# Kernel tuning notes

Hardware: AMD Instinct MI355X
Metric: run time of the kernel (lower is better)

## Reference

```python
import jax, jax.numpy as jnp
import numpy as np

NUM_T = 1000   # num_timesteps == timesteps -> skip = 1, seq = range(0, 1000)
ETA = 0.1
BETA_START, BETA_END = 1e-4, 0.02


def _ddim_schedule():
    # get_beta_schedule: linspace in float64, then cast
    betas = np.linspace(BETA_START, BETA_END, NUM_T, dtype=np.float64)
    # compute_alpha prepends beta=0 -> alpha_cumprod[0] = 1.0, indexed at t+1
    alph = np.concatenate([[1.0], np.cumprod(1.0 - betas)]).astype(np.float32)
    seq = np.arange(NUM_T)
    seq_next = np.concatenate([[-1], seq[:-1]])
    at = alph[seq + 1]
    at_next = alph[seq_next + 1]   # t=-1 -> alph[0] = 1.0
    # loop iterates reversed(seq) x reversed(seq_next)
    return (jnp.asarray(at[::-1].copy()),
            jnp.asarray(at_next[::-1].copy()),
            jnp.asarray(seq[::-1].copy(), dtype=jnp.int32))


def setup_inputs() -> dict:
    key = jax.random.key(0)
    k1, k2, k3, k4, k5 = jax.random.split(key, 5)
    n, c, s, h, w = 2, 3, 8, 64, 44
    return {
        "skes": jax.random.normal(k1, (n, c, s, h, w), dtype=jnp.float32),
        "sil_T": jax.random.normal(k2, (n * s, 1, h, w), dtype=jnp.float32),
        "w_skes": jax.random.normal(k3, (c,), dtype=jnp.float32),
        "w_sil": jax.random.normal(k4, (), dtype=jnp.float32),
        "t_scale": jax.random.normal(k5, (), dtype=jnp.float32),
    }


def reference(skes, sil_T, w_skes, w_sil, t_scale):
    n, c, s, h, w = skes.shape
    # rearrange 'n c s h w -> (n s) c h w'
    skes2 = jnp.transpose(skes, (0, 2, 1, 3, 4)).reshape(n * s, c, h, w)
    # surrogate denoiser condition: 1x1 channel projection of the skeleton maps
    cond = jnp.einsum('nchw,c->nhw', skes2, w_skes)[:, None]  # (n*s,1,h,w)
    at_r, atn_r, idx_r = _ddim_schedule()
    noise_key = jax.random.key(42)

    def model(sil_t, t_val):
        t_emb = t_scale * (t_val.astype(jnp.float32) / NUM_T)
        return jnp.tanh(cond + w_sil * sil_t + t_emb)

    def step(sil_t, x):
        at, atn, idx = x
        sil_0 = model(sil_t, idx)
        # NOTE: original uses the FIXED initial noise sil_T here (not sil_t)
        et = (sil_T - jnp.sqrt(at) * sil_0) / jnp.sqrt(1.0 - at)
        c1 = ETA * jnp.sqrt((1.0 - at / atn) * (1.0 - atn) / (1.0 - at))
        c2 = jnp.sqrt(jnp.maximum(1.0 - atn - c1 * c1, 0.0))
        noise = jax.random.normal(jax.random.fold_in(noise_key, idx),
                                  sil_T.shape, dtype=sil_T.dtype)
        sil_next = jnp.sqrt(atn) * sil_0 + c1 * noise + c2 * et
        return sil_next, sil_0

    _, preds = jax.lax.scan(step, sil_T, (at_r, atn_r, idx_r))
    # preds: (1000, n*s, 1, h, w) == stacked list of per-step sil_0 predictions
    return preds
```

## Files before the change

### kernel.cpp

```cpp
#include <hip/hip_runtime.h>
#include <cstdint>

#define NSTEP 1000
#define NELEM 45056
#define HW    2816
#define EPB   64
#define PW    7
#define BLK   ((PW + 1) * 64)
#define WIN   40
#define NWIN  (NSTEP / WIN)
#define NBUF  2
#define TABC_OFF 16384
#define WS_NEED  (TABC_OFF + NSTEP * 8)

struct AlphTab { float a[NSTEP + 1]; };

constexpr AlphTab make_alph() {
    AlphTab t{};
    t.a[0] = 1.0f;
    double alph = 1.0;
    const double start = 1e-4, stop = 0.02;
    const double step = (stop - start) / 999.0;
    for (int i = 0; i < NSTEP; ++i) {
        double beta = (i == NSTEP - 1) ? stop : ((double)i * step + start);
        alph *= (1.0 - beta);
        t.a[i + 1] = (float)alph;
    }
    return t;
}
constexpr AlphTab ALPH = make_alph();

__device__ __forceinline__ void tf20(uint32_t K0, uint32_t K1, uint32_t K2,
                                     uint32_t& x0, uint32_t& x1) {
    x0 += K0; x1 += K1;
#define TFR(r) { x0 += x1; x1 = ((x1 << r) | (x1 >> (32 - r))); x1 ^= x0; }
    TFR(13) TFR(15) TFR(26) TFR(6)
    x0 += K1; x1 += K2 + 1u;
    TFR(17) TFR(29) TFR(16) TFR(24)
    x0 += K2; x1 += K0 + 2u;
    TFR(13) TFR(15) TFR(26) TFR(6)
    x0 += K0; x1 += K1 + 3u;
    TFR(17) TFR(29) TFR(16) TFR(24)
    x0 += K1; x1 += K2 + 4u;
    TFR(13) TFR(15) TFR(26) TFR(6)
    x0 += K2; x1 += K0 + 5u;
#undef TFR
}

__device__ __forceinline__ float fast_tanh(float x) {
    const float e2 = __expf(x + x);
    const float r  = __builtin_amdgcn_rcpf(e2 + 1.0f);
    return fmaf(-2.0f, r, 1.0f);
}

__device__ __forceinline__ float bits_to_erfinv(uint32_t bits) {
    const float f2 = __uint_as_float((bits >> 9) | 0x3F800000u) - 1.0f;
    const float u  = f2 * 2.0f - 0.99999994f;
    const float t1 = (1.0f - u) * (1.0f + u);
    const float w  = __log2f(t1) * -0.6931472f;
    const bool  lt = w < 5.0f;

    const float wwn = w - 2.5f;
    float pn =           2.81022636e-08f;
    pn = fmaf(pn, wwn,   3.43273939e-07f);
    pn = fmaf(pn, wwn,  -3.5233877e-06f);
    pn = fmaf(pn, wwn,  -4.39150654e-06f);
    pn = fmaf(pn, wwn,   0.00021858087f);
    pn = fmaf(pn, wwn,  -0.00125372503f);
    pn = fmaf(pn, wwn,  -0.00417768164f);
    pn = fmaf(pn, wwn,   0.246640727f);
    pn = fmaf(pn, wwn,   1.50140941f);

    float p = pn;
    if (__any(!lt)) {
        const float sw  = __builtin_amdgcn_sqrtf(w);
        const float wwf = sw - 3.0f;
        float pf =           -0.000200214257f;
        pf = fmaf(pf, wwf,    0.000100950558f);
        pf = fmaf(pf, wwf,    0.00134934322f);
        pf = fmaf(pf, wwf,   -0.00367342844f);
        pf = fmaf(pf, wwf,    0.00573950773f);
        pf = fmaf(pf, wwf,   -0.0076224613f);
        pf = fmaf(pf, wwf,    0.00943887047f);
        pf = fmaf(pf, wwf,    1.00167406f);
        pf = fmaf(pf, wwf,    2.83297682f);
        p = lt ? pn : pf;
    }
    return p * u;
}

__global__ __launch_bounds__(256)
void setup_kernel(const float* __restrict__ tsc_p,
                  uint4* __restrict__ tabPg, uint2* __restrict__ tabCg) {
    const int k = (int)(blockIdx.x * 256u + threadIdx.x);
    if (k >= NSTEP) return;
    const float tsc = tsc_p[0];
    const float L2E2 = 2.8853900817779268f;
    const int t = 999 - k;
    const float at  = ALPH.a[t + 1];
    const float atn = ALPH.a[t];
    const float c1 = 0.1f * sqrtf((1.0f - at / atn) * (1.0f - atn) / (1.0f - at));
    const float c2 = sqrtf(fmaxf(1.0f - atn - c1 * c1, 0.0f));
    const float rs = 1.0f / sqrtf(1.0f - at);
    const float A  = sqrtf(atn) - c2 * sqrtf(at) * rs;
    const float e  = c2 * rs;
    const float temb = tsc * ((float)t / 1000.0f);
    uint32_t k0 = 0u, k1 = (uint32_t)t;
    tf20(0u, 42u, 0x1BD11BDAu ^ 42u, k0, k1);
    tabPg[k] = make_uint4(__float_as_uint(c1 * 1.4142135f),
                          __float_as_uint(e), k0, k1);
    tabCg[k] = make_uint2(__float_as_uint(A), __float_as_uint(temb * L2E2));
}

__device__ __forceinline__ void produce_window(const uint4* __restrict__ tabPg,
                                               float* __restrict__ db,
                                               int kbase, int wid, int lane,
                                               int j, float sT) {
    const int ks0 = __builtin_amdgcn_readfirstlane(kbase + wid);
#pragma unroll 2
    for (int s = 0, kk = wid; kk < WIN; ++s, kk += PW) {
        const uint4 ta = tabPg[ks0 + s * PW];
        uint32_t x0 = 0u, x1 = (uint32_t)j;
        tf20(ta.z, ta.w, ta.z ^ ta.w ^ 0x1BD11BDAu, x0, x1);
        const float ei = bits_to_erfinv(x0 ^ x1);
        db[kk * EPB + lane] =
            fmaf(__uint_as_float(ta.x), ei, __uint_as_float(ta.y) * sT);
    }
}

__global__ __launch_bounds__(BLK, 8)
void fused_kernel(const float* __restrict__ skes,
                  const float* __restrict__ silT,
                  const float* __restrict__ wskes,
                  const float* __restrict__ wsil_p,
                  const uint4* __restrict__ tabPg,
                  const uint2* __restrict__ tabCg,
                  float* __restrict__ out) {
    __shared__ __align__(16) float dbuf[NBUF][WIN][EPB];

    const int wid  = (int)(threadIdx.x >> 6);
    const int lane = (int)(threadIdx.x & 63);
    const int j    = (int)(blockIdx.x * EPB) + lane;

    const float sT = silT[j];

    float cc2 = 0.0f, ws2 = 0.0f, sil = 0.0f;
    if (wid == PW) {
        const float L2E2 = 2.8853900817779268f;
        const int ns = j / HW;
        const int hw = j - ns * HW;
        const int n  = ns >> 3;
        const int ss = ns & 7;
        const float* sk = skes + (size_t)((n * 3) * 8 + ss) * HW + hw;
        const float w0 = wskes[0], w1 = wskes[1], w2 = wskes[2];
        const float cond = fmaf(w2, sk[2 * 8 * HW], fmaf(w1, sk[8 * HW], w0 * sk[0]));
        cc2 = cond * L2E2;
        ws2 = wsil_p[0] * L2E2;
        sil = sT;
    }

    if (wid < PW) {
        produce_window(tabPg, &dbuf[0][0][0], 0, wid, lane, j, sT);
    }
    __syncthreads();

    float* op = out + j;

    for (int w = 0; w < NWIN; ++w) {
        if (wid < PW) {
            if (w + 1 < NWIN) {
                produce_window(tabPg, &dbuf[(w + 1) & (NBUF - 1)][0][0],
                               (w + 1) * WIN, wid, lane, j, sT);
            }
        } else {
            const float* db = &dbuf[w & (NBUF - 1)][0][0];
            const int ks0 = __builtin_amdgcn_readfirstlane(w * WIN);
#pragma unroll 1
            for (int g = 0; g < WIN / 8; ++g) {
                float d8[8]; uint2 t8[8];
#pragma unroll
                for (int i = 0; i < 8; ++i) {
                    d8[i] = db[(g * 8 + i) * EPB + lane];
                    t8[i] = tabCg[ks0 + g * 8 + i];
                }
#pragma unroll
                for (int i = 0; i < 8; ++i) {
                    const float A  = __uint_as_float(t8[i].x);
                    const float tb = __uint_as_float(t8[i].y);
                    const float e2 = __builtin_amdgcn_exp2f(fmaf(ws2, sil, cc2 + tb));
                    const float r  = __builtin_amdgcn_rcpf(e2 + 1.0f);
                    const float s0 = fmaf(-2.0f, r, 1.0f);
                    *op = s0; op += NELEM;
                    sil = fmaf(A, s0, d8[i]);
                }
            }
        }
        __syncthreads();
    }
}

__global__ __launch_bounds__(256)
void diffgait_mono(const float* __restrict__ skes,
                   const float* __restrict__ silT,
                   const float* __restrict__ wskes,
                   const float* __restrict__ wsil_p,
                   const float* __restrict__ tsc_p,
                   float* __restrict__ out) {
    __shared__ __align__(16) uint32_t tab[NSTEP][8];
    const float wsil = wsil_p[0];
    const float tsc  = tsc_p[0];
    for (int k = (int)threadIdx.x; k < NSTEP; k += 256) {
        const int t = 999 - k;
        const float at  = ALPH.a[t + 1];
        const float atn = ALPH.a[t];
        const float c1 = 0.1f * sqrtf((1.0f - at / atn) * (1.0f - atn) / (1.0f - at));
        const float c2 = sqrtf(fmaxf(1.0f - atn - c1 * c1, 0.0f));
        const float rs = 1.0f / sqrtf(1.0f - at);
        const float A  = sqrtf(atn) - c2 * sqrtf(at) * rs;
        const float e  = c2 * rs;
        const float temb = tsc * ((float)t / 1000.0f);
        uint32_t x0 = 0u, x1 = (uint32_t)t;
        tf20(0u, 42u, 0x1BD11BDAu ^ 42u, x0, x1);
        tab[k][0] = __float_as_uint(A);
        tab[k][1] = __float_as_uint(temb);
        tab[k][2] = __float_as_uint(c1 * 1.4142135f);
        tab[k][3] = __float_as_uint(e);
        tab[k][4] = x0;
        tab[k][5] = x1;
        tab[k][6] = x0 ^ x1 ^ 0x1BD11BDAu;
        tab[k][7] = 0u;
    }
    __syncthreads();
    const int j  = (int)(blockIdx.x * 256u + threadIdx.x);
    const int ns = j / HW;
    const int hw = j - ns * HW;
    const int n  = ns >> 3;
    const int ss = ns & 7;
    const float* sk = skes + (size_t)((n * 3) * 8 + ss) * HW + hw;
    const float w0 = wskes[0], w1 = wskes[1], w2 = wskes[2];
    const float cond = fmaf(w2, sk[2 * 8 * HW], fmaf(w1, sk[8 * HW], w0 * sk[0]));
    const float sT = silT[j];
    float sil = sT;
    float* op = out + j;
#pragma unroll 2
    for (int k = 0; k < NSTEP; ++k) {
        const uint4 ta = *(const uint4*)&tab[k][0];
        const uint4 tb = *(const uint4*)&tab[k][4];
        uint32_t x0 = 0u, x1 = (uint32_t)j;
        tf20(tb.x, tb.y, tb.z, x0, x1);
        const float ei = bits_to_erfinv(x0 ^ x1);
        const float d  = fmaf(__uint_as_float(ta.z), ei, __uint_as_float(ta.w) * sT);
        const float s0 = fast_tanh(fmaf(wsil, sil, cond) + __uint_as_float(ta.y));
        *op = s0; op += NELEM;
        sil = fmaf(__uint_as_float(ta.x), s0, d);
    }
}

extern "C" void kernel_launch(void* const* d_in, const int* in_sizes, int n_in,
                              void* d_out, int out_size, void* d_ws, size_t ws_size,
                              hipStream_t stream) {
    const float* skes = (const float*)d_in[0];
    const float* silT = (const float*)d_in[1];
    const float* wsk  = (const float*)d_in[2];
    const float* wsil = (const float*)d_in[3];
    const float* tsc  = (const float*)d_in[4];
    float* out = (float*)d_out;
    (void)in_sizes; (void)n_in; (void)out_size;

    if (ws_size >= (size_t)WS_NEED) {
        uint4* tabPg = (uint4*)d_ws;
        uint2* tabCg = (uint2*)((char*)d_ws + TABC_OFF);
        hipLaunchKernelGGL(setup_kernel, dim3(4), dim3(256), 0, stream,
                           tsc, tabPg, tabCg);
        dim3 grid(NELEM / EPB), block(BLK);
        hipLaunchKernelGGL(fused_kernel, grid, block, 0, stream,
                           skes, silT, wsk, wsil, tabPg, tabCg, out);
    } else {
        dim3 grid(NELEM / 256), block(256);
        hipLaunchKernelGGL(diffgait_mono, grid, block, 0, stream,
                           skes, silT, wsk, wsil, tsc, out);
    }
}
```

Measured before the change: 294.2 us.

## Replace producer/consumer warp split with round-robin windows chained via LDS flag

The kernel used to dedicate seven warps to generating noise into a double-buffered LDS window while one warp ran the serial recurrence. Now all five warps own windows round-robin. Each warp computes its own window's noise into registers, spins on a volatile LDS flag until the previous window's final state arrives, runs the serial recurrence at raised priority, then hands the state on through LDS. This removes the block-wide barriers and spreads the recurrence across warps. In exchange it relies on spin-waiting through volatile shared memory without fences, uses more registers for the noise array, and drops the occupancy hint.

```diff
diff --git a/kernel.cpp b/kernel.cpp
--- a/kernel.cpp
+++ b/kernel.cpp
@@ -4,12 +4,11 @@
 #define NSTEP 1000
 #define NELEM 45056
 #define HW    2816
-#define EPB   64
-#define PW    7
-#define BLK   ((PW + 1) * 64)
-#define WIN   40
+#define WPG   5
+#define WIN   20
 #define NWIN  (NSTEP / WIN)
-#define NBUF  2
+#define SPW   (NWIN / WPG)
+#define BLK   (WPG * 64)
 #define TABC_OFF 16384
 #define WS_NEED  (TABC_OFF + NSTEP * 8)
 
@@ -112,23 +111,7 @@
     tabCg[k] = make_uint2(__float_as_uint(A), __float_as_uint(temb * L2E2));
 }
 
-__device__ __forceinline__ void produce_window(const uint4* __restrict__ tabPg,
-                                               float* __restrict__ db,
-                                               int kbase, int wid, int lane,
-                                               int j, float sT) {
-    const int ks0 = __builtin_amdgcn_readfirstlane(kbase + wid);
-#pragma unroll 2
-    for (int s = 0, kk = wid; kk < WIN; ++s, kk += PW) {
-        const uint4 ta = tabPg[ks0 + s * PW];
-        uint32_t x0 = 0u, x1 = (uint32_t)j;
-        tf20(ta.z, ta.w, ta.z ^ ta.w ^ 0x1BD11BDAu, x0, x1);
-        const float ei = bits_to_erfinv(x0 ^ x1);
-        db[kk * EPB + lane] =
-            fmaf(__uint_as_float(ta.x), ei, __uint_as_float(ta.y) * sT);
-    }
-}
-
-__global__ __launch_bounds__(BLK, 8)
+__global__ __launch_bounds__(BLK)
 void fused_kernel(const float* __restrict__ skes,
                   const float* __restrict__ silT,
                   const float* __restrict__ wskes,
@@ -136,66 +119,71 @@
                   const uint4* __restrict__ tabPg,
                   const uint2* __restrict__ tabCg,
                   float* __restrict__ out) {
-    __shared__ __align__(16) float dbuf[NBUF][WIN][EPB];
+    __shared__ float    lds_sil[64];
+    __shared__ uint32_t flag;
 
     const int wid  = (int)(threadIdx.x >> 6);
     const int lane = (int)(threadIdx.x & 63);
-    const int j    = (int)(blockIdx.x * EPB) + lane;
-
+    const int j    = (int)(blockIdx.x * 64u) + lane;
+
+    if (threadIdx.x == 0) flag = 0u;
+
+    const float L2E2 = 2.8853900817779268f;
     const float sT = silT[j];
-
-    float cc2 = 0.0f, ws2 = 0.0f, sil = 0.0f;
-    if (wid == PW) {
-        const float L2E2 = 2.8853900817779268f;
-        const int ns = j / HW;
-        const int hw = j - ns * HW;
-        const int n  = ns >> 3;
-        const int ss = ns & 7;
-        const float* sk = skes + (size_t)((n * 3) * 8 + ss) * HW + hw;
-        const float w0 = wskes[0], w1 = wskes[1], w2 = wskes[2];
-        const float cond = fmaf(w2, sk[2 * 8 * HW], fmaf(w1, sk[8 * HW], w0 * sk[0]));
-        cc2 = cond * L2E2;
-        ws2 = wsil_p[0] * L2E2;
-        sil = sT;
-    }
-
-    if (wid < PW) {
-        produce_window(tabPg, &dbuf[0][0][0], 0, wid, lane, j, sT);
-    }
+    const int ns = j / HW;
+    const int hw = j - ns * HW;
+    const int n  = ns >> 3;
+    const int ss = ns & 7;
+    const float* sk = skes + (size_t)((n * 3) * 8 + ss) * HW + hw;
+    const float w0 = wskes[0], w1 = wskes[1], w2 = wskes[2];
+    const float cond = fmaf(w2, sk[2 * 8 * HW], fmaf(w1, sk[8 * HW], w0 * sk[0]));
+    const float cc2 = cond * L2E2;
+    const float ws2 = wsil_p[0] * L2E2;
+
     __syncthreads();
 
+    volatile uint32_t* vflag = &flag;
     float* op = out + j;
 
-    for (int w = 0; w < NWIN; ++w) {
-        if (wid < PW) {
-            if (w + 1 < NWIN) {
-                produce_window(tabPg, &dbuf[(w + 1) & (NBUF - 1)][0][0],
-                               (w + 1) * WIN, wid, lane, j, sT);
-            }
-        } else {
-            const float* db = &dbuf[w & (NBUF - 1)][0][0];
-            const int ks0 = __builtin_amdgcn_readfirstlane(w * WIN);
 #pragma unroll 1
-            for (int g = 0; g < WIN / 8; ++g) {
-                float d8[8]; uint2 t8[8];
+    for (int s = 0; s < SPW; ++s) {
+        const int w  = s * WPG + wid;
+        const int kb = w * WIN;
+        const int ks0 = __builtin_amdgcn_readfirstlane(kb);
+
+        float nz[WIN];
 #pragma unroll
-                for (int i = 0; i < 8; ++i) {
-                    d8[i] = db[(g * 8 + i) * EPB + lane];
-                    t8[i] = tabCg[ks0 + g * 8 + i];
-                }
+        for (int kk = 0; kk < WIN; ++kk) {
+            const uint4 ta = tabPg[ks0 + kk];
+            uint32_t x0 = 0u, x1 = (uint32_t)j;
+            tf20(ta.z, ta.w, ta.z ^ ta.w ^ 0x1BD11BDAu, x0, x1);
+            const float ei = bits_to_erfinv(x0 ^ x1);
+            nz[kk] = fmaf(__uint_as_float(ta.x), ei, __uint_as_float(ta.y) * sT);
+        }
+
+        while (*vflag < (uint32_t)w) __builtin_amdgcn_s_sleep(1);
+        asm volatile("" ::: "memory");
+        float sil = (w == 0) ? sT : lds_sil[lane];
+
+        __builtin_amdgcn_s_setprio(1);
+        float* opw = op + (size_t)kb * NELEM;
 #pragma unroll
-                for (int i = 0; i < 8; ++i) {
-                    const float A  = __uint_as_float(t8[i].x);
-                    const float tb = __uint_as_float(t8[i].y);
-                    const float e2 = __builtin_amdgcn_exp2f(fmaf(ws2, sil, cc2 + tb));
-                    const float r  = __builtin_amdgcn_rcpf(e2 + 1.0f);
-                    const float s0 = fmaf(-2.0f, r, 1.0f);
-                    *op = s0; op += NELEM;
-                    sil = fmaf(A, s0, d8[i]);
-                }
-            }
+        for (int kk = 0; kk < WIN; ++kk) {
+            const uint2 tt = tabCg[ks0 + kk];
+            const float A  = __uint_as_float(tt.x);
+            const float tb = __uint_as_float(tt.y);
+            const float e2 = __builtin_amdgcn_exp2f(fmaf(ws2, sil, cc2 + tb));
+            const float r  = __builtin_amdgcn_rcpf(e2 + 1.0f);
+            const float s0 = fmaf(-2.0f, r, 1.0f);
+            opw[(size_t)kk * NELEM] = s0;
+            sil = fmaf(A, s0, nz[kk]);
         }
-        __syncthreads();
+        __builtin_amdgcn_s_setprio(0);
+
+        lds_sil[lane] = sil;
+        asm volatile("" ::: "memory");
+        *vflag = (uint32_t)(w + 1);
+        asm volatile("" ::: "memory");
     }
 }
 
@@ -272,7 +260,7 @@
         uint2* tabCg = (uint2*)((char*)d_ws + TABC_OFF);
         hipLaunchKernelGGL(setup_kernel, dim3(4), dim3(256), 0, stream,
                            tsc, tabPg, tabCg);
-        dim3 grid(NELEM / EPB), block(BLK);
+        dim3 grid(NELEM / 64), block(BLK);
         hipLaunchKernelGGL(fused_kernel, grid, block, 0, stream,
                            skes, silT, wsk, wsil, tabPg, tabCg, out);
     } else {
```

Measured after the change: 308.4 us. 4.8% more time.
